# Kernel optimization log

Measured on AMD Instinct MI355X. Metric: run time of the kernel, lower is better.

The kernel has to match this reference:

```python
import jax, jax.numpy as jnp
import numpy as np

B, S, D, H = 32, 512, 512, 1024  # batch, seq, latents_dims, hidden (=prod(out_dims))


def setup_inputs() -> dict:
    key = jax.random.key(0)
    ks = jax.random.split(key, 7)
    scale_ih = 1.0 / np.sqrt(D)
    scale_hh = 1.0 / np.sqrt(H)
    return {
        "x": jax.random.normal(ks[0], (B, S, D), dtype=jnp.float32),
        "h0": jax.random.uniform(ks[1], (B, H), dtype=jnp.float32),
        "c0": jax.random.uniform(ks[2], (B, H), dtype=jnp.float32),
        "W_ih": jax.random.normal(ks[3], (4 * H, D), dtype=jnp.float32) * scale_ih,
        "W_hh": jax.random.normal(ks[4], (4 * H, H), dtype=jnp.float32) * scale_hh,
        "b_ih": jax.random.normal(ks[5], (4 * H,), dtype=jnp.float32) * scale_hh,
        "b_hh": jax.random.normal(ks[6], (4 * H,), dtype=jnp.float32) * scale_hh,
    }


def reference(x, h0, c0, W_ih, W_hh, b_ih, b_hh):
    # Single-layer LSTM, PyTorch gate order (i, f, g, o).
    # Precompute the input projection for all timesteps in one GEMM: [B,S,4H]
    x_proj = jnp.einsum("bsd,gd->bsg", x, W_ih) + b_ih + b_hh
    xs = jnp.swapaxes(x_proj, 0, 1)  # [S, B, 4H]

    def step(carry, xp_t):
        h, c = carry  # [B, H] each
        gates = xp_t + h @ W_hh.T  # [B, 4H]
        i, f, g, o = jnp.split(gates, 4, axis=-1)
        i = jax.nn.sigmoid(i)
        f = jax.nn.sigmoid(f)
        g = jnp.tanh(g)
        o = jax.nn.sigmoid(o)
        c = f * c + i * g
        h = o * jnp.tanh(c)
        return (h, c), h

    _, hs = jax.lax.scan(step, (h0, c0), xs)  # hs: [S, B, H]
    out = jnp.swapaxes(hs, 0, 1)  # [B, S, H]
    # view(*x.shape[:2], *out_dims) with out_dims=[1024] is a no-op reshape
    return out.reshape(B, S, H)
```

## Files before the change

### kernel.cpp

```cpp
#include <hip/hip_runtime.h>

typedef __bf16 bf16_t;
typedef __bf16 bf16x8 __attribute__((ext_vector_type(8)));
typedef __bf16 bf16x4 __attribute__((ext_vector_type(4)));
typedef __bf16 bf16x2 __attribute__((ext_vector_type(2)));
typedef float f32x16 __attribute__((ext_vector_type(16)));
typedef int i32x4 __attribute__((ext_vector_type(4)));

#define SZ_XBF    (16384ull*512*2)
#define SZ_WIH    (4096ull*512*2)
#define SZ_WHH    (4096ull*1024*2)
#define SZ_XPROJ  (16384ull*4096*2)
#define SZ_HTR    (513ull*32*1024*2)
#define OFF_XBF   (0ull)
#define OFF_WIH   (OFF_XBF + SZ_XBF)
#define OFF_WHH   (OFF_WIH + SZ_WIH)
#define OFF_XPROJ (OFF_WHH + SZ_WHH)
#define OFF_HTR   (OFF_XPROJ + SZ_XPROJ)


__global__ __launch_bounds__(256) void convert_pack(
    const float* __restrict__ x, const float* __restrict__ h0,
    const float* __restrict__ Wih, const float* __restrict__ Whh,
    bf16_t* __restrict__ xbf, bf16_t* __restrict__ wihbf,
    bf16_t* __restrict__ whhbf, bf16_t* __restrict__ htr)
{
  long long v = (long long)blockIdx.x * 256 + threadIdx.x;
  if (v < 2097152LL) {
    long long fi = v * 4;
    int b = (int)(fi >> 18);
    int rem = (int)(fi & 0x3FFFF);
    int s = rem >> 9, d = rem & 511;
    float4 f = *(const float4*)(x + fi);
    bf16x4 o; o.x = (bf16_t)f.x; o.y = (bf16_t)f.y; o.z = (bf16_t)f.z; o.w = (bf16_t)f.w;
    *(bf16x4*)(xbf + ((long long)(s*32 + b)*512 + d)) = o;
  } else if (v < 2621440LL) {
    long long fi = (v - 2097152LL) * 4;
    float4 f = *(const float4*)(Wih + fi);
    bf16x4 o; o.x = (bf16_t)f.x; o.y = (bf16_t)f.y; o.z = (bf16_t)f.z; o.w = (bf16_t)f.w;
    *(bf16x4*)(wihbf + fi) = o;
  } else if (v < 3670016LL) {
    long long fi = (v - 2621440LL) * 4;
    float4 f = *(const float4*)(Whh + fi);
    bf16x4 o; o.x = (bf16_t)f.x; o.y = (bf16_t)f.y; o.z = (bf16_t)f.z; o.w = (bf16_t)f.w;
    *(bf16x4*)(whhbf + fi) = o;
  } else if (v < 3678208LL) {
    long long fi = (v - 3670016LL) * 4;
    int b = (int)(fi >> 10), c = (int)(fi & 1023);
    float4 f = *(const float4*)(h0 + fi);
    bf16x4 o; o.x = (bf16_t)f.x; o.y = (bf16_t)f.y; o.z = (bf16_t)f.z; o.w = (bf16_t)f.w;
    *(bf16x4*)(htr + (long long)(c >> 4) * 512 + b * 16 + (c & 15)) = o;
  } else if (v < 5775360LL) {
    long long idx = v - 3678208LL;
    *(int4*)(htr + 32768LL + idx * 8) = make_int4(-1, -1, -1, -1);
  }
}

__global__ __launch_bounds__(256) void xproj_gemm(
    const bf16_t* __restrict__ Xb, const bf16_t* __restrict__ Wb,
    const float* __restrict__ bih, const float* __restrict__ bhh,
    bf16_t* __restrict__ XP)
{
  __shared__ bf16_t As[128*64];
  __shared__ bf16_t Bs[128*64];
  const int tid = threadIdx.x;
  const int lane = tid & 63, wave = tid >> 6;
  const int mhalf = wave & 1, nhalf = wave >> 1;
  const int l31 = lane & 31, khi = lane >> 5;
  const int m0 = blockIdx.x * 128, n0 = blockIdx.y * 128;

  f32x16 acc[2][2] = {};

  for (int kb = 0; kb < 8; ++kb) {
    const int k0 = kb * 64;
    __syncthreads();
#pragma unroll
    for (int j = 0; j < 4; ++j) {
      int cid = j * 256 + tid;
      int r = cid >> 3, bs = cid & 7;
      int bb = bs ^ (r & 7);
      *(bf16x8*)(As + cid * 8) = *(const bf16x8*)(Xb + (long long)(m0 + r) * 512 + k0 + bb * 8);
      *(bf16x8*)(Bs + cid * 8) = *(const bf16x8*)(Wb + (long long)(n0 + r) * 512 + k0 + bb * 8);
    }
    __syncthreads();
#pragma unroll
    for (int ks = 0; ks < 4; ++ks) {
      int blk = ks * 2 + khi;
      bf16x8 af[2], bfr[2];
#pragma unroll
      for (int mt = 0; mt < 2; ++mt) {
        int r = mhalf * 64 + mt * 32 + l31;
        af[mt] = *(const bf16x8*)(As + (r * 8 + (blk ^ (r & 7))) * 8);
      }
#pragma unroll
      for (int nt = 0; nt < 2; ++nt) {
        int r = nhalf * 64 + nt * 32 + l31;
        bfr[nt] = *(const bf16x8*)(Bs + (r * 8 + (blk ^ (r & 7))) * 8);
      }
#pragma unroll
      for (int mt = 0; mt < 2; ++mt)
#pragma unroll
        for (int nt = 0; nt < 2; ++nt)
          acc[mt][nt] = __builtin_amdgcn_mfma_f32_32x32x16_bf16(af[mt], bfr[nt], acc[mt][nt], 0, 0, 0);
    }
  }
#pragma unroll
  for (int nt = 0; nt < 2; ++nt) {
    int ng = n0 + nhalf * 64 + nt * 32 + l31;
    float bias = bih[ng] + bhh[ng];
#pragma unroll
    for (int mt = 0; mt < 2; ++mt) {
#pragma unroll
      for (int r = 0; r < 16; ++r) {
        int row = (r & 3) + 8 * (r >> 2) + 4 * khi;
        long long mg = m0 + mhalf * 64 + mt * 32 + row;
        XP[mg * 4096 + ng] = (bf16_t)(acc[mt][nt][r] + bias);
      }
    }
  }
}

__device__ __forceinline__ float sigf(float x) { return 1.0f / (1.0f + __expf(-x)); }
__device__ __forceinline__ float tanhfast(float x) {
  float e = __expf(-2.0f * fabsf(x));
  float t = (1.0f - e) / (1.0f + e);
  return copysignf(t, x);
}
__device__ __forceinline__ unsigned umax2(unsigned a, unsigned b) { return a > b ? a : b; }
__device__ __forceinline__ unsigned umax4(i32x4 v) {
  return umax2(umax2((unsigned)v[0], (unsigned)v[1]),
               umax2((unsigned)v[2], (unsigned)v[3]));
}

#define LD16(dst, ptr, OFF) \
  asm volatile("global_load_dwordx4 %0, %1, off offset:" OFF " sc0 sc1" \
               : "=v"(dst) : "v"(ptr) : "memory")

__global__ __launch_bounds__(256, 1) void lstm_rec(
    const bf16_t* __restrict__ Whh_b, const bf16_t* __restrict__ XP,
    const float* __restrict__ c0, float* __restrict__ OUT,
    bf16_t* __restrict__ HTR)
{
  const int tid = threadIdx.x;
  const int lane = tid & 63, wave = tid >> 6;
  const int kq = wave;
  const int wg = blockIdx.x;
  const int l31 = lane & 31, khi = lane >> 5;

  const int g0row = (l31 >> 4) * 1024 + wg * 16 + (l31 & 15);
  const int g1row = (2 + (l31 >> 4)) * 1024 + wg * 16 + (l31 & 15);
  const int kqb = kq * 256 + khi * 8;
  bf16x8 w0[16], w1[16];
#pragma unroll
  for (int s = 0; s < 16; ++s) {
    w0[s] = *(const bf16x8*)(Whh_b + (long long)g0row * 1024 + kqb + s * 16);
    w1[s] = *(const bf16x8*)(Whh_b + (long long)g1row * 1024 + kqb + s * 16);
  }

  const char* abase = (const char*)HTR + kq * 16384 + l31 * 32 + khi * 16;

  __shared__ float gLb[2][4][32][65];
  const int m_e = tid >> 3;
  const int jp = (tid & 7) * 2;
  float cr0 = c0[m_e * 1024 + wg * 16 + jp];
  float cr1 = c0[m_e * 1024 + wg * 16 + jp + 1];

  float xp[4][2];
  {
    const bf16_t* xpb = XP + (long long)m_e * 4096 + wg * 16 + jp;
#pragma unroll
    for (int g = 0; g < 4; ++g) {
      bf16x2 v = *(const bf16x2*)(xpb + g * 1024);
      xp[g][0] = (float)v.x; xp[g][1] = (float)v.y;
    }
  }

  float po0 = 0.0f, po1 = 0.0f;

  for (int t = 0; t < 512; ++t) {
    const char* p0 = abase + ((long long)t << 16);
    const char* p1 = p0 + 4096;
    const char* p2 = p0 + 8192;
    const char* p3 = p0 + 12288;
    i32x4 a[16];
    for (;;) {
      LD16(a[0],  p0, "0"); LD16(a[1],  p0, "1024"); LD16(a[2],  p0, "2048"); LD16(a[3],  p0, "3072");
      LD16(a[4],  p1, "0"); LD16(a[5],  p1, "1024"); LD16(a[6],  p1, "2048"); LD16(a[7],  p1, "3072");
      LD16(a[8],  p2, "0"); LD16(a[9],  p2, "1024"); LD16(a[10], p2, "2048"); LD16(a[11], p2, "3072");
      LD16(a[12], p3, "0"); LD16(a[13], p3, "1024"); LD16(a[14], p3, "2048"); LD16(a[15], p3, "3072");
      asm volatile("s_waitcnt vmcnt(0)" ::: "memory");
      __builtin_amdgcn_sched_barrier(0);
      unsigned mA = 0, mB = 0, mC = 0, mD = 0;
#pragma unroll
      for (int s = 0; s < 16; s += 4) {
        mA = umax2(mA, umax4(a[s]));
        mB = umax2(mB, umax4(a[s + 1]));
        mC = umax2(mC, umax4(a[s + 2]));
        mD = umax2(mD, umax4(a[s + 3]));
      }
      unsigned mx = umax2(umax2(mA, mB), umax2(mC, mD));
      if (!__any((int)(mx == 0xFFFFFFFFu))) break;
    }

    if (t > 0)
      *(float2*)(OUT + ((long long)m_e * 512 + (t - 1)) * 1024 + wg * 16 + jp) =
          make_float2(po0, po1);

    f32x16 acc0 = {}, acc1 = {};
#pragma unroll
    for (int s = 0; s < 16; ++s) {
      bf16x8 af = __builtin_bit_cast(bf16x8, a[s]);
      acc0 = __builtin_amdgcn_mfma_f32_32x32x16_bf16(af, w0[s], acc0, 0, 0, 0);
      acc1 = __builtin_amdgcn_mfma_f32_32x32x16_bf16(af, w1[s], acc1, 0, 0, 0);
    }

    float (*gp)[65] = gLb[t & 1][kq];
#pragma unroll
    for (int r = 0; r < 16; ++r) {
      int mm = (r & 3) + 8 * (r >> 2) + 4 * khi;
      gp[mm][l31]      = acc0[r];
      gp[mm][32 + l31] = acc1[r];
    }
    __syncthreads();

    float (*ge)[32][65] = gLb[t & 1];
    float hv[2];
    {
      float ir  = ge[0][m_e][jp]      + ge[1][m_e][jp]      + ge[2][m_e][jp]      + ge[3][m_e][jp]      + xp[0][0];
      float fr  = ge[0][m_e][16 + jp] + ge[1][m_e][16 + jp] + ge[2][m_e][16 + jp] + ge[3][m_e][16 + jp] + xp[1][0];
      float gr  = ge[0][m_e][32 + jp] + ge[1][m_e][32 + jp] + ge[2][m_e][32 + jp] + ge[3][m_e][32 + jp] + xp[2][0];
      float orr = ge[0][m_e][48 + jp] + ge[1][m_e][48 + jp] + ge[2][m_e][48 + jp] + ge[3][m_e][48 + jp] + xp[3][0];
      float c = sigf(fr) * cr0 + sigf(ir) * tanhfast(gr);
      cr0 = c;
      hv[0] = sigf(orr) * tanhfast(c);
    }
    {
      int j = jp + 1;
      float ir  = ge[0][m_e][j]      + ge[1][m_e][j]      + ge[2][m_e][j]      + ge[3][m_e][j]      + xp[0][1];
      float fr  = ge[0][m_e][16 + j] + ge[1][m_e][16 + j] + ge[2][m_e][16 + j] + ge[3][m_e][16 + j] + xp[1][1];
      float gr  = ge[0][m_e][32 + j] + ge[1][m_e][32 + j] + ge[2][m_e][32 + j] + ge[3][m_e][32 + j] + xp[2][1];
      float orr = ge[0][m_e][48 + j] + ge[1][m_e][48 + j] + ge[2][m_e][48 + j] + ge[3][m_e][48 + j] + xp[3][1];
      float c = sigf(fr) * cr1 + sigf(ir) * tanhfast(gr);
      cr1 = c;
      hv[1] = sigf(orr) * tanhfast(c);
    }

    {
      bf16x2 h2; h2.x = (bf16_t)hv[0]; h2.y = (bf16_t)hv[1];
      unsigned int u = __builtin_bit_cast(unsigned int, h2);
      unsigned int* dst = (unsigned int*)(HTR + (long long)(t + 1) * 32768 +
                                          (long long)wg * 512 + m_e * 16 + jp);
      __hip_atomic_store(dst, u, __ATOMIC_RELAXED, __HIP_MEMORY_SCOPE_AGENT);
    }
    po0 = hv[0]; po1 = hv[1];

    if (t < 511) {
      const bf16_t* xpb = XP + ((long long)(t + 1) * 32 + m_e) * 4096 + wg * 16 + jp;
#pragma unroll
      for (int g = 0; g < 4; ++g) {
        bf16x2 v = *(const bf16x2*)(xpb + g * 1024);
        xp[g][0] = (float)v.x; xp[g][1] = (float)v.y;
      }
    }
  }
  *(float2*)(OUT + ((long long)m_e * 512 + 511) * 1024 + wg * 16 + jp) =
      make_float2(po0, po1);
}

extern "C" void kernel_launch(void* const* d_in, const int* in_sizes, int n_in,
                              void* d_out, int out_size, void* d_ws, size_t ws_size,
                              hipStream_t stream)
{
  const float* x   = (const float*)d_in[0];
  const float* h0  = (const float*)d_in[1];
  const float* c0  = (const float*)d_in[2];
  const float* Wih = (const float*)d_in[3];
  const float* Whh = (const float*)d_in[4];
  const float* bih = (const float*)d_in[5];
  const float* bhh = (const float*)d_in[6];
  float* out = (float*)d_out;

  char* ws = (char*)d_ws;
  bf16_t* xbf   = (bf16_t*)(ws + OFF_XBF);
  bf16_t* wihbf = (bf16_t*)(ws + OFF_WIH);
  bf16_t* whhbf = (bf16_t*)(ws + OFF_WHH);
  bf16_t* xproj = (bf16_t*)(ws + OFF_XPROJ);
  bf16_t* htr   = (bf16_t*)(ws + OFF_HTR);

  convert_pack<<<22560, 256, 0, stream>>>(x, h0, Wih, Whh, xbf, wihbf, whhbf, htr);
  xproj_gemm<<<dim3(128, 32), 256, 0, stream>>>(xbf, wihbf, bih, bhh, xproj);
  lstm_rec<<<64, 256, 0, stream>>>(whhbf, xproj, c0, out, htr);
}
```

Before: 1.530 ms.

## Repartition LSTM recurrence into 32 blocks of 8 waves splitting K eight ways

Halves the number of persistent recurrent workgroups from 64 to 32. Each workgroup now owns 32 hidden units across all four gates and uses 8 waves, each covering a 128-wide K slice. The aim is to reduce the number of blocks that must synchronise through global memory each timestep and to halve the per-wave polling load. The cost is more partial sums to reduce in LDS, a single-buffered LDS tile that needs an extra __syncthreads per step, and more register pressure from the 4 gate accumulators.

```diff
diff --git a/kernel.cpp b/kernel.cpp
--- a/kernel.cpp
+++ b/kernel.cpp
@@ -136,38 +136,38 @@
   asm volatile("global_load_dwordx4 %0, %1, off offset:" OFF " sc0 sc1" \
                : "=v"(dst) : "v"(ptr) : "memory")
 
-__global__ __launch_bounds__(256, 1) void lstm_rec(
+__global__ __launch_bounds__(512, 1) void lstm_rec(
     const bf16_t* __restrict__ Whh_b, const bf16_t* __restrict__ XP,
     const float* __restrict__ c0, float* __restrict__ OUT,
     bf16_t* __restrict__ HTR)
 {
   const int tid = threadIdx.x;
   const int lane = tid & 63, wave = tid >> 6;
-  const int kq = wave;
+  const int ke = wave;
   const int wg = blockIdx.x;
   const int l31 = lane & 31, khi = lane >> 5;
 
-  const int g0row = (l31 >> 4) * 1024 + wg * 16 + (l31 & 15);
-  const int g1row = (2 + (l31 >> 4)) * 1024 + wg * 16 + (l31 & 15);
-  const int kqb = kq * 256 + khi * 8;
-  bf16x8 w0[16], w1[16];
-#pragma unroll
-  for (int s = 0; s < 16; ++s) {
-    w0[s] = *(const bf16x8*)(Whh_b + (long long)g0row * 1024 + kqb + s * 16);
-    w1[s] = *(const bf16x8*)(Whh_b + (long long)g1row * 1024 + kqb + s * 16);
-  }
-
-  const char* abase = (const char*)HTR + kq * 16384 + l31 * 32 + khi * 16;
-
-  __shared__ float gLb[2][4][32][65];
-  const int m_e = tid >> 3;
-  const int jp = (tid & 7) * 2;
-  float cr0 = c0[m_e * 1024 + wg * 16 + jp];
-  float cr1 = c0[m_e * 1024 + wg * 16 + jp + 1];
+  const int kb8 = ke * 128 + khi * 8;
+  bf16x8 wr0[8], wr1[8], wr2[8], wr3[8];
+#pragma unroll
+  for (int s = 0; s < 8; ++s) {
+    wr0[s] = *(const bf16x8*)(Whh_b + (long long)(0 * 1024 + wg * 32 + l31) * 1024 + kb8 + s * 16);
+    wr1[s] = *(const bf16x8*)(Whh_b + (long long)(1 * 1024 + wg * 32 + l31) * 1024 + kb8 + s * 16);
+    wr2[s] = *(const bf16x8*)(Whh_b + (long long)(2 * 1024 + wg * 32 + l31) * 1024 + kb8 + s * 16);
+    wr3[s] = *(const bf16x8*)(Whh_b + (long long)(3 * 1024 + wg * 32 + l31) * 1024 + kb8 + s * 16);
+  }
+
+  const char* abase = (const char*)HTR + ke * 8192 + l31 * 32 + khi * 16;
+
+  __shared__ float gL[8][32][129];
+  const int m_e = tid >> 4;
+  const int jp = (tid & 15) * 2;
+  float cr0 = c0[m_e * 1024 + wg * 32 + jp];
+  float cr1 = c0[m_e * 1024 + wg * 32 + jp + 1];
 
   float xp[4][2];
   {
-    const bf16_t* xpb = XP + (long long)m_e * 4096 + wg * 16 + jp;
+    const bf16_t* xpb = XP + (long long)m_e * 4096 + wg * 32 + jp;
 #pragma unroll
     for (int g = 0; g < 4; ++g) {
       bf16x2 v = *(const bf16x2*)(xpb + g * 1024);
@@ -180,90 +180,84 @@
   for (int t = 0; t < 512; ++t) {
     const char* p0 = abase + ((long long)t << 16);
     const char* p1 = p0 + 4096;
-    const char* p2 = p0 + 8192;
-    const char* p3 = p0 + 12288;
-    i32x4 a[16];
+    i32x4 a[8];
     for (;;) {
-      LD16(a[0],  p0, "0"); LD16(a[1],  p0, "1024"); LD16(a[2],  p0, "2048"); LD16(a[3],  p0, "3072");
-      LD16(a[4],  p1, "0"); LD16(a[5],  p1, "1024"); LD16(a[6],  p1, "2048"); LD16(a[7],  p1, "3072");
-      LD16(a[8],  p2, "0"); LD16(a[9],  p2, "1024"); LD16(a[10], p2, "2048"); LD16(a[11], p2, "3072");
-      LD16(a[12], p3, "0"); LD16(a[13], p3, "1024"); LD16(a[14], p3, "2048"); LD16(a[15], p3, "3072");
+      LD16(a[0], p0, "0"); LD16(a[1], p0, "1024"); LD16(a[2], p0, "2048"); LD16(a[3], p0, "3072");
+      LD16(a[4], p1, "0"); LD16(a[5], p1, "1024"); LD16(a[6], p1, "2048"); LD16(a[7], p1, "3072");
       asm volatile("s_waitcnt vmcnt(0)" ::: "memory");
       __builtin_amdgcn_sched_barrier(0);
-      unsigned mA = 0, mB = 0, mC = 0, mD = 0;
-#pragma unroll
-      for (int s = 0; s < 16; s += 4) {
-        mA = umax2(mA, umax4(a[s]));
-        mB = umax2(mB, umax4(a[s + 1]));
-        mC = umax2(mC, umax4(a[s + 2]));
-        mD = umax2(mD, umax4(a[s + 3]));
-      }
+      unsigned mA = umax2(umax4(a[0]), umax4(a[1]));
+      unsigned mB = umax2(umax4(a[2]), umax4(a[3]));
+      unsigned mC = umax2(umax4(a[4]), umax4(a[5]));
+      unsigned mD = umax2(umax4(a[6]), umax4(a[7]));
       unsigned mx = umax2(umax2(mA, mB), umax2(mC, mD));
       if (!__any((int)(mx == 0xFFFFFFFFu))) break;
     }
 
     if (t > 0)
-      *(float2*)(OUT + ((long long)m_e * 512 + (t - 1)) * 1024 + wg * 16 + jp) =
+      *(float2*)(OUT + ((long long)m_e * 512 + (t - 1)) * 1024 + wg * 32 + jp) =
           make_float2(po0, po1);
 
-    f32x16 acc0 = {}, acc1 = {};
-#pragma unroll
-    for (int s = 0; s < 16; ++s) {
+    f32x16 acc0 = {}, acc1 = {}, acc2 = {}, acc3 = {};
+#pragma unroll
+    for (int s = 0; s < 8; ++s) {
       bf16x8 af = __builtin_bit_cast(bf16x8, a[s]);
-      acc0 = __builtin_amdgcn_mfma_f32_32x32x16_bf16(af, w0[s], acc0, 0, 0, 0);
-      acc1 = __builtin_amdgcn_mfma_f32_32x32x16_bf16(af, w1[s], acc1, 0, 0, 0);
-    }
-
-    float (*gp)[65] = gLb[t & 1][kq];
+      acc0 = __builtin_amdgcn_mfma_f32_32x32x16_bf16(af, wr0[s], acc0, 0, 0, 0);
+      acc1 = __builtin_amdgcn_mfma_f32_32x32x16_bf16(af, wr1[s], acc1, 0, 0, 0);
+      acc2 = __builtin_amdgcn_mfma_f32_32x32x16_bf16(af, wr2[s], acc2, 0, 0, 0);
+      acc3 = __builtin_amdgcn_mfma_f32_32x32x16_bf16(af, wr3[s], acc3, 0, 0, 0);
+    }
+
+    float (*gp)[129] = gL[ke];
 #pragma unroll
     for (int r = 0; r < 16; ++r) {
       int mm = (r & 3) + 8 * (r >> 2) + 4 * khi;
       gp[mm][l31]      = acc0[r];
       gp[mm][32 + l31] = acc1[r];
-    }
-    __syncthreads();
-
-    float (*ge)[32][65] = gLb[t & 1];
+      gp[mm][64 + l31] = acc2[r];
+      gp[mm][96 + l31] = acc3[r];
+    }
+    __syncthreads();
+
     float hv[2];
-    {
-      float ir  = ge[0][m_e][jp]      + ge[1][m_e][jp]      + ge[2][m_e][jp]      + ge[3][m_e][jp]      + xp[0][0];
-      float fr  = ge[0][m_e][16 + jp] + ge[1][m_e][16 + jp] + ge[2][m_e][16 + jp] + ge[3][m_e][16 + jp] + xp[1][0];
-      float gr  = ge[0][m_e][32 + jp] + ge[1][m_e][32 + jp] + ge[2][m_e][32 + jp] + ge[3][m_e][32 + jp] + xp[2][0];
-      float orr = ge[0][m_e][48 + jp] + ge[1][m_e][48 + jp] + ge[2][m_e][48 + jp] + ge[3][m_e][48 + jp] + xp[3][0];
-      float c = sigf(fr) * cr0 + sigf(ir) * tanhfast(gr);
-      cr0 = c;
-      hv[0] = sigf(orr) * tanhfast(c);
-    }
-    {
-      int j = jp + 1;
-      float ir  = ge[0][m_e][j]      + ge[1][m_e][j]      + ge[2][m_e][j]      + ge[3][m_e][j]      + xp[0][1];
-      float fr  = ge[0][m_e][16 + j] + ge[1][m_e][16 + j] + ge[2][m_e][16 + j] + ge[3][m_e][16 + j] + xp[1][1];
-      float gr  = ge[0][m_e][32 + j] + ge[1][m_e][32 + j] + ge[2][m_e][32 + j] + ge[3][m_e][32 + j] + xp[2][1];
-      float orr = ge[0][m_e][48 + j] + ge[1][m_e][48 + j] + ge[2][m_e][48 + j] + ge[3][m_e][48 + j] + xp[3][1];
-      float c = sigf(fr) * cr1 + sigf(ir) * tanhfast(gr);
-      cr1 = c;
-      hv[1] = sigf(orr) * tanhfast(c);
+#pragma unroll
+    for (int e = 0; e < 2; ++e) {
+      int j = jp + e;
+      float ir  = xp[0][e], fr = xp[1][e], gr = xp[2][e], orr = xp[3][e];
+#pragma unroll
+      for (int k = 0; k < 8; ++k) {
+        ir  += gL[k][m_e][j];
+        fr  += gL[k][m_e][32 + j];
+        gr  += gL[k][m_e][64 + j];
+        orr += gL[k][m_e][96 + j];
+      }
+      float cprev = e ? cr1 : cr0;
+      float c = sigf(fr) * cprev + sigf(ir) * tanhfast(gr);
+      if (e) cr1 = c; else cr0 = c;
+      hv[e] = sigf(orr) * tanhfast(c);
     }
 
     {
       bf16x2 h2; h2.x = (bf16_t)hv[0]; h2.y = (bf16_t)hv[1];
       unsigned int u = __builtin_bit_cast(unsigned int, h2);
       unsigned int* dst = (unsigned int*)(HTR + (long long)(t + 1) * 32768 +
-                                          (long long)wg * 512 + m_e * 16 + jp);
+                                          (long long)(2 * wg + (jp >> 4)) * 512 +
+                                          m_e * 16 + (jp & 15));
       __hip_atomic_store(dst, u, __ATOMIC_RELAXED, __HIP_MEMORY_SCOPE_AGENT);
     }
     po0 = hv[0]; po1 = hv[1];
 
     if (t < 511) {
-      const bf16_t* xpb = XP + ((long long)(t + 1) * 32 + m_e) * 4096 + wg * 16 + jp;
+      const bf16_t* xpb = XP + ((long long)(t + 1) * 32 + m_e) * 4096 + wg * 32 + jp;
 #pragma unroll
       for (int g = 0; g < 4; ++g) {
         bf16x2 v = *(const bf16x2*)(xpb + g * 1024);
         xp[g][0] = (float)v.x; xp[g][1] = (float)v.y;
       }
     }
-  }
-  *(float2*)(OUT + ((long long)m_e * 512 + 511) * 1024 + wg * 16 + jp) =
+    __syncthreads();
+  }
+  *(float2*)(OUT + ((long long)m_e * 512 + 511) * 1024 + wg * 32 + jp) =
       make_float2(po0, po1);
 }
 
@@ -289,5 +283,5 @@
 
   convert_pack<<<22560, 256, 0, stream>>>(x, h0, Wih, Whh, xbf, wihbf, whhbf, htr);
   xproj_gemm<<<dim3(128, 32), 256, 0, stream>>>(xbf, wihbf, bih, bhh, xproj);
-  lstm_rec<<<64, 256, 0, stream>>>(whhbf, xproj, c0, out, htr);
-}
+  lstm_rec<<<32, 512, 0, stream>>>(whhbf, xproj, c0, out, htr);
+}
```

Result: slower. 2.059 ms (+34.5%).

## Track per-chunk readiness of h and overlap MFMA with polling reloads

Applied to the files above, without the earlier changes.

The spin-wait on the previous step's hidden state now tracks which of the 16 chunks are ready (no sentinel value) and reloads only the chunks still pending. MFMAs for ready chunks are issued inside the poll loop so matrix work overlaps the wait for the remaining chunks. The cost is more branching, per-chunk wave votes and divergent control flow in the hot recurrence loop. It may also upset register allocation or scheduling around the inline-asm loads.

```diff
diff --git a/kernel.cpp b/kernel.cpp
--- a/kernel.cpp
+++ b/kernel.cpp
@@ -183,36 +183,54 @@
     const char* p2 = p0 + 8192;
     const char* p3 = p0 + 12288;
     i32x4 a[16];
+    f32x16 acc0 = {}, acc1 = {};
+    LD16(a[0],  p0, "0"); LD16(a[1],  p0, "1024"); LD16(a[2],  p0, "2048"); LD16(a[3],  p0, "3072");
+    LD16(a[4],  p1, "0"); LD16(a[5],  p1, "1024"); LD16(a[6],  p1, "2048"); LD16(a[7],  p1, "3072");
+    LD16(a[8],  p2, "0"); LD16(a[9],  p2, "1024"); LD16(a[10], p2, "2048"); LD16(a[11], p2, "3072");
+    LD16(a[12], p3, "0"); LD16(a[13], p3, "1024"); LD16(a[14], p3, "2048"); LD16(a[15], p3, "3072");
+    unsigned done = 0u;
     for (;;) {
-      LD16(a[0],  p0, "0"); LD16(a[1],  p0, "1024"); LD16(a[2],  p0, "2048"); LD16(a[3],  p0, "3072");
-      LD16(a[4],  p1, "0"); LD16(a[5],  p1, "1024"); LD16(a[6],  p1, "2048"); LD16(a[7],  p1, "3072");
-      LD16(a[8],  p2, "0"); LD16(a[9],  p2, "1024"); LD16(a[10], p2, "2048"); LD16(a[11], p2, "3072");
-      LD16(a[12], p3, "0"); LD16(a[13], p3, "1024"); LD16(a[14], p3, "2048"); LD16(a[15], p3, "3072");
       asm volatile("s_waitcnt vmcnt(0)" ::: "memory");
       __builtin_amdgcn_sched_barrier(0);
-      unsigned mA = 0, mB = 0, mC = 0, mD = 0;
-#pragma unroll
-      for (int s = 0; s < 16; s += 4) {
-        mA = umax2(mA, umax4(a[s]));
-        mB = umax2(mB, umax4(a[s + 1]));
-        mC = umax2(mC, umax4(a[s + 2]));
-        mD = umax2(mD, umax4(a[s + 3]));
-      }
-      unsigned mx = umax2(umax2(mA, mB), umax2(mC, mD));
-      if (!__any((int)(mx == 0xFFFFFFFFu))) break;
+      unsigned newly = 0u;
+#pragma unroll
+      for (int s = 0; s < 16; ++s)
+        if (!((done >> s) & 1u))
+          if (!__any((int)(umax4(a[s]) == 0xFFFFFFFFu)))
+            newly |= 1u << s;
+      done |= newly;
+      const bool last = (done == 0xFFFFu);
+      if (!last) {
+        if (!((done >>  0) & 1u)) LD16(a[0],  p0, "0");
+        if (!((done >>  1) & 1u)) LD16(a[1],  p0, "1024");
+        if (!((done >>  2) & 1u)) LD16(a[2],  p0, "2048");
+        if (!((done >>  3) & 1u)) LD16(a[3],  p0, "3072");
+        if (!((done >>  4) & 1u)) LD16(a[4],  p1, "0");
+        if (!((done >>  5) & 1u)) LD16(a[5],  p1, "1024");
+        if (!((done >>  6) & 1u)) LD16(a[6],  p1, "2048");
+        if (!((done >>  7) & 1u)) LD16(a[7],  p1, "3072");
+        if (!((done >>  8) & 1u)) LD16(a[8],  p2, "0");
+        if (!((done >>  9) & 1u)) LD16(a[9],  p2, "1024");
+        if (!((done >> 10) & 1u)) LD16(a[10], p2, "2048");
+        if (!((done >> 11) & 1u)) LD16(a[11], p2, "3072");
+        if (!((done >> 12) & 1u)) LD16(a[12], p3, "0");
+        if (!((done >> 13) & 1u)) LD16(a[13], p3, "1024");
+        if (!((done >> 14) & 1u)) LD16(a[14], p3, "2048");
+        if (!((done >> 15) & 1u)) LD16(a[15], p3, "3072");
+      }
+#pragma unroll
+      for (int s = 0; s < 16; ++s)
+        if ((newly >> s) & 1u) {
+          bf16x8 af = __builtin_bit_cast(bf16x8, a[s]);
+          acc0 = __builtin_amdgcn_mfma_f32_32x32x16_bf16(af, w0[s], acc0, 0, 0, 0);
+          acc1 = __builtin_amdgcn_mfma_f32_32x32x16_bf16(af, w1[s], acc1, 0, 0, 0);
+        }
+      if (last) break;
     }
 
     if (t > 0)
       *(float2*)(OUT + ((long long)m_e * 512 + (t - 1)) * 1024 + wg * 16 + jp) =
           make_float2(po0, po1);
-
-    f32x16 acc0 = {}, acc1 = {};
-#pragma unroll
-    for (int s = 0; s < 16; ++s) {
-      bf16x8 af = __builtin_bit_cast(bf16x8, a[s]);
-      acc0 = __builtin_amdgcn_mfma_f32_32x32x16_bf16(af, w0[s], acc0, 0, 0, 0);
-      acc1 = __builtin_amdgcn_mfma_f32_32x32x16_bf16(af, w1[s], acc1, 0, 0, 0);
-    }
 
     float (*gp)[65] = gLb[t & 1][kq];
 #pragma unroll
```

Result: slower. 1.792 ms (+17.1%).

## Double-buffer the polling loads of the hidden state in the LSTM recurrence

Applied to the files above, without the earlier changes.

The per-step spin-wait that loads the previous hidden state and checks it for the not-ready sentinel now keeps two rounds of 16 loads in flight, in buffers a and b. It waits only for the older round (vmcnt(16)), validates it, and reissues into that buffer while the other round is still outstanding. The idea is to cut the round-trip latency of each polling iteration in this latency-bound serial loop. The store of the previous step's output also moves ahead of the poll so it overlaps with the loads. In exchange it uses more vector registers, adds extra memory traffic while spinning, and leaves stale loads in flight that the next step's wait counts must account for.

```diff
diff --git a/kernel.cpp b/kernel.cpp
--- a/kernel.cpp
+++ b/kernel.cpp
@@ -136,6 +136,35 @@
   asm volatile("global_load_dwordx4 %0, %1, off offset:" OFF " sc0 sc1" \
                : "=v"(dst) : "v"(ptr) : "memory")
 
+#define ISSUE_ROUND(buf) do { \
+  LD16(buf[0],  p0, "0"); LD16(buf[1],  p0, "1024"); LD16(buf[2],  p0, "2048"); LD16(buf[3],  p0, "3072"); \
+  LD16(buf[4],  p1, "0"); LD16(buf[5],  p1, "1024"); LD16(buf[6],  p1, "2048"); LD16(buf[7],  p1, "3072"); \
+  LD16(buf[8],  p2, "0"); LD16(buf[9],  p2, "1024"); LD16(buf[10], p2, "2048"); LD16(buf[11], p2, "3072"); \
+  LD16(buf[12], p3, "0"); LD16(buf[13], p3, "1024"); LD16(buf[14], p3, "2048"); LD16(buf[15], p3, "3072"); \
+} while (0)
+
+#define VALID16(buf, ok) do { \
+  unsigned mA = umax2(umax4(buf[0]),  umax4(buf[1])); \
+  unsigned mB = umax2(umax4(buf[2]),  umax4(buf[3])); \
+  mA = umax2(mA, umax2(umax4(buf[4]),  umax4(buf[5]))); \
+  mB = umax2(mB, umax2(umax4(buf[6]),  umax4(buf[7]))); \
+  unsigned mC = umax2(umax4(buf[8]),  umax4(buf[9])); \
+  unsigned mD = umax2(umax4(buf[10]), umax4(buf[11])); \
+  mC = umax2(mC, umax2(umax4(buf[12]), umax4(buf[13]))); \
+  mD = umax2(mD, umax2(umax4(buf[14]), umax4(buf[15]))); \
+  unsigned mx = umax2(umax2(mA, mB), umax2(mC, mD)); \
+  ok = !__any((int)(mx == 0xFFFFFFFFu)); \
+} while (0)
+
+#define MFMA16(buf) do { \
+  _Pragma("unroll") \
+  for (int s = 0; s < 16; ++s) { \
+    bf16x8 af = __builtin_bit_cast(bf16x8, buf[s]); \
+    acc0 = __builtin_amdgcn_mfma_f32_32x32x16_bf16(af, w0[s], acc0, 0, 0, 0); \
+    acc1 = __builtin_amdgcn_mfma_f32_32x32x16_bf16(af, w1[s], acc1, 0, 0, 0); \
+  } \
+} while (0)
+
 __global__ __launch_bounds__(256, 1) void lstm_rec(
     const bf16_t* __restrict__ Whh_b, const bf16_t* __restrict__ XP,
     const float* __restrict__ c0, float* __restrict__ OUT,
@@ -176,43 +205,38 @@
   }
 
   float po0 = 0.0f, po1 = 0.0f;
+  i32x4 a[16], b[16];
 
   for (int t = 0; t < 512; ++t) {
+    if (t > 0)
+      *(float2*)(OUT + ((long long)m_e * 512 + (t - 1)) * 1024 + wg * 16 + jp) =
+          make_float2(po0, po1);
+
     const char* p0 = abase + ((long long)t << 16);
     const char* p1 = p0 + 4096;
     const char* p2 = p0 + 8192;
     const char* p3 = p0 + 12288;
-    i32x4 a[16];
+
+    asm volatile("s_waitcnt vmcnt(10)" ::: "memory");
+    ISSUE_ROUND(a);
+    ISSUE_ROUND(b);
+
+    bool useA = true;
     for (;;) {
-      LD16(a[0],  p0, "0"); LD16(a[1],  p0, "1024"); LD16(a[2],  p0, "2048"); LD16(a[3],  p0, "3072");
-      LD16(a[4],  p1, "0"); LD16(a[5],  p1, "1024"); LD16(a[6],  p1, "2048"); LD16(a[7],  p1, "3072");
-      LD16(a[8],  p2, "0"); LD16(a[9],  p2, "1024"); LD16(a[10], p2, "2048"); LD16(a[11], p2, "3072");
-      LD16(a[12], p3, "0"); LD16(a[13], p3, "1024"); LD16(a[14], p3, "2048"); LD16(a[15], p3, "3072");
-      asm volatile("s_waitcnt vmcnt(0)" ::: "memory");
+      asm volatile("s_waitcnt vmcnt(16)" ::: "memory");
       __builtin_amdgcn_sched_barrier(0);
-      unsigned mA = 0, mB = 0, mC = 0, mD = 0;
-#pragma unroll
-      for (int s = 0; s < 16; s += 4) {
-        mA = umax2(mA, umax4(a[s]));
-        mB = umax2(mB, umax4(a[s + 1]));
-        mC = umax2(mC, umax4(a[s + 2]));
-        mD = umax2(mD, umax4(a[s + 3]));
-      }
-      unsigned mx = umax2(umax2(mA, mB), umax2(mC, mD));
-      if (!__any((int)(mx == 0xFFFFFFFFu))) break;
-    }
-
-    if (t > 0)
-      *(float2*)(OUT + ((long long)m_e * 512 + (t - 1)) * 1024 + wg * 16 + jp) =
-          make_float2(po0, po1);
+      bool ok; VALID16(a, ok);
+      if (ok) { useA = true; break; }
+      ISSUE_ROUND(a);
+      asm volatile("s_waitcnt vmcnt(16)" ::: "memory");
+      __builtin_amdgcn_sched_barrier(0);
+      VALID16(b, ok);
+      if (ok) { useA = false; break; }
+      ISSUE_ROUND(b);
+    }
 
     f32x16 acc0 = {}, acc1 = {};
-#pragma unroll
-    for (int s = 0; s < 16; ++s) {
-      bf16x8 af = __builtin_bit_cast(bf16x8, a[s]);
-      acc0 = __builtin_amdgcn_mfma_f32_32x32x16_bf16(af, w0[s], acc0, 0, 0, 0);
-      acc1 = __builtin_amdgcn_mfma_f32_32x32x16_bf16(af, w1[s], acc1, 0, 0, 0);
-    }
+    if (useA) { MFMA16(a); } else { MFMA16(b); }
 
     float (*gp)[65] = gLb[t & 1][kq];
 #pragma unroll
```

New measurement: 1.777 ms. +16.1%, slower.
